# Performance work log

Hardware: AMD Instinct MI355X
Metric: run time of the kernel (lower is better)

The kernel has to match this reference:

```python
import jax, jax.numpy as jnp
import numpy as np

B, S, D = 32, 2048, 8
H = 256
COUPLING = -1.0  # TC['WOBBLE_COUPLING'] default
WOBBLE_STEP = 0.03125


def setup_inputs() -> dict:
    key = jax.random.key(0)
    k = jax.random.split(key, 5)
    return {
        'x': jax.random.normal(k[0], (B, S, D), dtype=jnp.float32),
        'We': jax.random.normal(k[1], (H, D), dtype=jnp.float32) * 0.35,
        'be': jax.random.normal(k[2], (H,), dtype=jnp.float32) * 0.02,
        'Wr': jax.random.normal(k[3], (256, 7 * H), dtype=jnp.float32) * 0.02,
        'br': jax.random.normal(k[4], (256,), dtype=jnp.float32) * 0.02,
    }


def _forward(x, We, be, Wr, br):
    Bm, Sm, _ = x.shape
    h = We.shape[0]

    def step(carry, xt):
        ph, wb, prev_xt, has_prev = carry
        pt = xt @ We.T + be                      # [B,h] embedded phase increments
        # xpt = stack([cos(pt), sin(pt)]); accumulator consumes the spinor pair,
        # equivalent to the wrapped phase delta atan2(sin, cos)
        delta = jnp.arctan2(jnp.sin(pt), jnp.cos(pt))
        wb2 = wb + WOBBLE_STEP
        is_rep = has_prev * jnp.all(xt == prev_xt, axis=1, keepdims=True).astype(x.dtype)
        # WobblePhaseAccumulator(spinor=True): phase advances by delta plus
        # coupling-modulated wobble; wobble channel accumulates delta
        ph_out = ph + delta + COUPLING * jnp.sin(wb2)
        wb_out = wb2 + delta
        ph_new = ph_out
        wb_new = is_rep * wb_out + (1.0 - is_rep) * wb2
        ph_s = 0.5 * ph_new
        readout = jnp.concatenate([
            jnp.cos(ph_new), jnp.sin(ph_new),
            jnp.cos(ph_s), jnp.sin(ph_s),
            jnp.cos(wb_new), jnp.sin(wb_new),
            ph_new,
        ], axis=1)                                # [B, 7h]
        logits = readout @ Wr.T + br              # [B, 256]
        return (ph_new, wb_new, xt, jnp.ones((), x.dtype)), (logits, ph_new, wb_new)

    ph0 = jnp.zeros((Bm, h), x.dtype)
    wb0 = jnp.zeros((Bm, h), x.dtype)
    prev0 = jnp.zeros((Bm, x.shape[2]), x.dtype)
    carry0 = (ph0, wb0, prev0, jnp.zeros((), x.dtype))
    xs = jnp.swapaxes(x, 0, 1)                    # [S,B,D]
    _, (logits, ph_hist, wb_hist) = jax.lax.scan(step, carry0, xs)
    logits = jnp.swapaxes(logits, 0, 1)           # [B,S,256]
    ph_hist = jnp.swapaxes(ph_hist, 0, 1)         # [B,S,h]
    wb_hist = jnp.swapaxes(wb_hist, 0, 1)         # [B,S,h]
    return logits, ph_hist, wb_hist


def reference(x, We, be, Wr, br):
    return _forward(x, We, be, Wr, br)
```

## Files before the change

### kernel.cpp

```cpp
#include <hip/hip_runtime.h>
#include <hip/hip_bf16.h>
#include <math.h>

#define NB 32
#define NS 2048
#define ND 8
#define NH 256
#define NK 1792
#define NO 256
#define NM (NB*NS)
#define WSTEP 0.03125f
#define CCH 64
#define LCH (NS/CCH)

typedef __attribute__((ext_vector_type(8))) short short8;
typedef __attribute__((ext_vector_type(4))) float f32x4;

__device__ float g_ssum[NB*CCH*NH];
__device__ float g_wb0 [NB*CCH*NH];
__device__ float g_esum[NB*CCH*NH];
__device__ float g_ph0 [NB*CCH*NH];
__device__ float g_rep [NB*NS];
__device__ unsigned short g_bb[NO*NK];

__device__ __forceinline__ unsigned short bf16_rn(float f){
    union { float f; unsigned int u; } v; v.f = f;
    unsigned int u = v.u;
    unsigned int r = (u + 0x7FFFu + ((u >> 16) & 1u)) >> 16;
    return (unsigned short)r;
}

extern "C" __global__ __launch_bounds__(256)
void k_delta(const float* __restrict__ x, const float* __restrict__ We,
             const float* __restrict__ be, float* __restrict__ delta){
    int blk = blockIdx.x;
    int b = blk >> 6;
    int c = blk & (CCH-1);
    int t0 = c * LCH;
    int h = threadIdx.x;
    __shared__ float xs[(LCH+1)*ND];
    __shared__ float rep[LCH];

    for(int i = h; i < (LCH+1)*ND/4; i += 256){
        int row  = i >> 1;
        int col4 = (i & 1) * 4;
        int t = t0 - 1 + row; if(t < 0) t = 0;
        *(float4*)&xs[row*ND + col4] = *(const float4*)&x[((size_t)b*NS + t)*ND + col4];
    }
    __syncthreads();
    if(h < LCH){
        int t = t0 + h;
        float fl = 0.f;
        if(t > 0){
            bool eq = true;
            #pragma unroll
            for(int d2 = 0; d2 < ND; ++d2) eq = eq && (xs[(h+1)*ND+d2] == xs[h*ND+d2]);
            fl = eq ? 1.f : 0.f;
        }
        rep[h] = fl;
        g_rep[b*NS + t] = fl;
    }
    __syncthreads();

    float4 w0 = *(const float4*)&We[h*ND];
    float4 w1 = *(const float4*)&We[h*ND + 4];
    float bh = be[h];
    float ssum = 0.f;
    for(int j = 0; j < LCH; ++j){
        const float* xr = &xs[(j+1)*ND];
        float pt = bh + xr[0]*w0.x + xr[1]*w0.y + xr[2]*w0.z + xr[3]*w0.w
                      + xr[4]*w1.x + xr[5]*w1.y + xr[6]*w1.z + xr[7]*w1.w;
        float s, cc;
        sincosf(pt, &s, &cc);
        float d = atan2f(s, cc);
        delta[((size_t)(t0+j)*NB + b)*NH + h] = d;
        ssum += WSTEP + rep[j]*d;
    }
    g_ssum[(b*CCH + c)*NH + h] = ssum;
}

extern "C" __global__ __launch_bounds__(256)
void k_prefix_s(){
    int g = blockIdx.x*256 + threadIdx.x;
    int b = g >> 8, h = g & 255;
    float acc = 0.f;
    for(int c = 0; c < CCH; ++c){
        size_t idx = ((size_t)(b*CCH + c))*NH + h;
        g_wb0[idx] = acc;
        acc += g_ssum[idx];
    }
}
extern "C" __global__ __launch_bounds__(256)
void k_prefix_e(){
    int g = blockIdx.x*256 + threadIdx.x;
    int b = g >> 8, h = g & 255;
    float acc = 0.f;
    for(int c = 0; c < CCH; ++c){
        size_t idx = ((size_t)(b*CCH + c))*NH + h;
        g_ph0[idx] = acc;
        acc += g_esum[idx];
    }
}

extern "C" __global__ __launch_bounds__(256)
void k_escan(const float* __restrict__ delta, float* __restrict__ wb_hist){
    int blk = blockIdx.x;
    int b = blk >> 6, c = blk & (CCH-1), t0 = c*LCH, h = threadIdx.x;
    __shared__ float rep[LCH];
    if(h < LCH) rep[h] = g_rep[b*NS + t0 + h];
    __syncthreads();
    float wb = g_wb0[(b*CCH + c)*NH + h];
    const float* dp = delta + (size_t)t0*NB*NH + b*NH + h;
    float* wp = wb_hist + ((size_t)b*NS + t0)*NH + h;
    float d[LCH];
    #pragma unroll
    for(int j = 0; j < LCH; ++j) d[j] = dp[(size_t)j*(NB*NH)];
    float esum = 0.f;
    #pragma unroll
    for(int j = 0; j < LCH; ++j){
        float wb2 = wb + WSTEP;
        float e = d[j] - sinf(wb2);
        esum += e;
        wb = wb2 + rep[j]*d[j];
        wp[(size_t)j*NH] = wb;
    }
    g_esum[(b*CCH + c)*NH + h] = esum;
}

extern "C" __global__ __launch_bounds__(256)
void k_phw(const float* __restrict__ delta, float* __restrict__ ph_hist){
    int blk = blockIdx.x;
    int b = blk >> 6, c = blk & (CCH-1), t0 = c*LCH, h = threadIdx.x;
    __shared__ float rep[LCH];
    if(h < LCH) rep[h] = g_rep[b*NS + t0 + h];
    __syncthreads();
    float wb = g_wb0[(b*CCH + c)*NH + h];
    float ph = g_ph0[(b*CCH + c)*NH + h];
    const float* dp = delta + (size_t)t0*NB*NH + b*NH + h;
    float* pp = ph_hist + ((size_t)b*NS + t0)*NH + h;
    float d[LCH];
    #pragma unroll
    for(int j = 0; j < LCH; ++j) d[j] = dp[(size_t)j*(NB*NH)];
    #pragma unroll
    for(int j = 0; j < LCH; ++j){
        float wb2 = wb + WSTEP;
        float e = d[j] - sinf(wb2);
        ph += e;
        wb = wb2 + rep[j]*d[j];
        pp[(size_t)j*NH] = ph;
    }
}

extern "C" __global__ __launch_bounds__(256)
void k_bconv(const float* __restrict__ Wr){
    int i = (blockIdx.x*256 + threadIdx.x) * 8;
    if(i >= NO*NK) return;
    float4 a = *(const float4*)&Wr[i];
    float4 b = *(const float4*)&Wr[i+4];
    union { unsigned int u[4]; uint4 v; } r;
    r.u[0] = (unsigned int)bf16_rn(a.x) | ((unsigned int)bf16_rn(a.y) << 16);
    r.u[1] = (unsigned int)bf16_rn(a.z) | ((unsigned int)bf16_rn(a.w) << 16);
    r.u[2] = (unsigned int)bf16_rn(b.x) | ((unsigned int)bf16_rn(b.y) << 16);
    r.u[3] = (unsigned int)bf16_rn(b.z) | ((unsigned int)bf16_rn(b.w) << 16);
    *(uint4*)&g_bb[i] = r.v;
}

extern "C" __global__ __launch_bounds__(512, 4)
void k_logits(const float* __restrict__ ph_hist, const float* __restrict__ wb_hist,
              const float* __restrict__ br, float* __restrict__ logits){
    __shared__ __align__(16) unsigned short Al[128][40];
    int tid  = threadIdx.x;
    int m0   = blockIdx.x * 128;
    int lane = tid & 63, wid = tid >> 6;
    int wm = wid >> 2, wn = wid & 3;
    int l15 = lane & 15, kg = lane >> 4;
    int colb = wn*64 + l15;
    int arow = tid >> 2, ah = (tid & 3) * 8;

    f32x4 acc[4][4];
    f32x4 zz = {0.f, 0.f, 0.f, 0.f};
    #pragma unroll
    for(int i = 0; i < 4; ++i)
        #pragma unroll
        for(int j = 0; j < 4; ++j) acc[i][j] = zz;

    for(int ks = 0; ks < 56; ++ks){
        int c    = ks >> 3;
        int kcol = (ks & 7) * 32;

        const float* src = (c == 4 || c == 5) ? wb_hist : ph_hist;
        const float* p = src + (size_t)(m0 + arow)*NH + kcol + ah;
        float4 x0 = *(const float4*)p;
        float4 x1 = *(const float4*)(p + 4);
        float v[8] = {x0.x, x0.y, x0.z, x0.w, x1.x, x1.y, x1.z, x1.w};
        if(c != 6){
            float sc = (c == 2 || c == 3) ? 0.07957747154594767f
                                          : 0.15915494309189535f;
            bool is_sin = (c & 1);
            #pragma unroll
            for(int j = 0; j < 8; ++j){
                float r = v[j] * sc;
                r -= floorf(r);
                v[j] = is_sin ? __builtin_amdgcn_sinf(r) : __builtin_amdgcn_cosf(r);
            }
        }
        union { unsigned int u[4]; uint4 q; } pk;
        #pragma unroll
        for(int j = 0; j < 4; ++j)
            asm("v_cvt_pk_bf16_f32 %0, %1, %2"
                : "=v"(pk.u[j]) : "v"(v[2*j]), "v"(v[2*j+1]));

        short8 bfr[4];
        #pragma unroll
        for(int nf = 0; nf < 4; ++nf)
            bfr[nf] = *(const short8*)&g_bb[(size_t)(colb + nf*16)*NK + c*256 + kcol + kg*8];

        __syncthreads();
        *(uint4*)&Al[arow][ah] = pk.q;
        __syncthreads();

        short8 afr[4];
        #pragma unroll
        for(int mf = 0; mf < 4; ++mf)
            afr[mf] = *(const short8*)&Al[wm*64 + mf*16 + l15][kg*8];
        #pragma unroll
        for(int mf = 0; mf < 4; ++mf)
            #pragma unroll
            for(int nf = 0; nf < 4; ++nf)
                acc[mf][nf] = __builtin_amdgcn_mfma_f32_16x16x32_bf16(
                    afr[mf], bfr[nf], acc[mf][nf], 0, 0, 0);
    }

    #pragma unroll
    for(int nf = 0; nf < 4; ++nf){
        int col = wn*64 + nf*16 + l15;
        float bias = br[col];
        #pragma unroll
        for(int mf = 0; mf < 4; ++mf){
            int row = m0 + wm*64 + mf*16 + kg*4;
            #pragma unroll
            for(int r = 0; r < 4; ++r)
                logits[(size_t)(row + r)*NO + col] = acc[mf][nf][r] + bias;
        }
    }
}

extern "C" void kernel_launch(void* const* d_in, const int* in_sizes, int n_in,
                              void* d_out, int out_size, void* d_ws, size_t ws_size,
                              hipStream_t stream){
    const float* x  = (const float*)d_in[0];
    const float* We = (const float*)d_in[1];
    const float* be = (const float*)d_in[2];
    const float* Wr = (const float*)d_in[3];
    const float* br = (const float*)d_in[4];

    float* logits = (float*)d_out;
    float* ph     = logits + (size_t)NM*NO;
    float* wb     = ph + (size_t)NM*NH;
    float* delta  = logits;

    hipLaunchKernelGGL(k_bconv,    dim3((NO*NK/8 + 255)/256), dim3(256), 0, stream, Wr);
    hipLaunchKernelGGL(k_delta,    dim3(NB*CCH), dim3(256), 0, stream, x, We, be, delta);
    hipLaunchKernelGGL(k_prefix_s, dim3(32),     dim3(256), 0, stream);
    hipLaunchKernelGGL(k_escan,    dim3(NB*CCH), dim3(256), 0, stream, delta, wb);
    hipLaunchKernelGGL(k_prefix_e, dim3(32),     dim3(256), 0, stream);
    hipLaunchKernelGGL(k_phw,      dim3(NB*CCH), dim3(256), 0, stream, delta, ph);
    hipLaunchKernelGGL(k_logits,   dim3(NM/128), dim3(512), 0, stream, ph, wb, br, logits);
}
```

Baseline: 415.4 us.

## Fuse readout feature build per h-slice and use double-angle identities

The logits kernel now loops over 8 h-slices instead of 56 k-steps. Each slice loads ph and wb once, computes sin/cos of ph/2 and derives cos/sin of ph with double-angle identities, then writes all 7 feature blocks to a wider LDS tile before running the MFMAs. This cuts redundant global reloads of ph_hist (four reads per element become one), halves the transcendental count for the ph features, and drops barriers from 112 to 16 per block. In exchange LDS use per block grows and register pressure rises, which may reduce occupancy under the (512,4) launch bounds. The double-angle values also round slightly differently from direct evaluation.

New measurement: 400.8 us. 1.04x faster.

```diff
diff --git a/kernel.cpp b/kernel.cpp
--- a/kernel.cpp
+++ b/kernel.cpp
@@ -165,17 +165,18 @@
     *(uint4*)&g_bb[i] = r.v;
 }
 
+#define LSTR 232
 extern "C" __global__ __launch_bounds__(512, 4)
 void k_logits(const float* __restrict__ ph_hist, const float* __restrict__ wb_hist,
               const float* __restrict__ br, float* __restrict__ logits){
-    __shared__ __align__(16) unsigned short Al[128][40];
+    __shared__ __align__(16) unsigned short Al[128][LSTR];
     int tid  = threadIdx.x;
     int m0   = blockIdx.x * 128;
     int lane = tid & 63, wid = tid >> 6;
     int wm = wid >> 2, wn = wid & 3;
     int l15 = lane & 15, kg = lane >> 4;
     int colb = wn*64 + l15;
-    int arow = tid >> 2, ah = (tid & 3) * 8;
+    int arow = tid >> 2, aq = (tid & 3) * 8;
 
     f32x4 acc[4][4];
     f32x4 zz = {0.f, 0.f, 0.f, 0.f};
@@ -184,51 +185,81 @@
         #pragma unroll
         for(int j = 0; j < 4; ++j) acc[i][j] = zz;
 
-    for(int ks = 0; ks < 56; ++ks){
-        int c    = ks >> 3;
-        int kcol = (ks & 7) * 32;
-
-        const float* src = (c == 4 || c == 5) ? wb_hist : ph_hist;
-        const float* p = src + (size_t)(m0 + arow)*NH + kcol + ah;
-        float4 x0 = *(const float4*)p;
-        float4 x1 = *(const float4*)(p + 4);
-        float v[8] = {x0.x, x0.y, x0.z, x0.w, x1.x, x1.y, x1.z, x1.w};
-        if(c != 6){
-            float sc = (c == 2 || c == 3) ? 0.07957747154594767f
-                                          : 0.15915494309189535f;
-            bool is_sin = (c & 1);
-            #pragma unroll
-            for(int j = 0; j < 8; ++j){
-                float r = v[j] * sc;
-                r -= floorf(r);
-                v[j] = is_sin ? __builtin_amdgcn_sinf(r) : __builtin_amdgcn_cosf(r);
-            }
-        }
-        union { unsigned int u[4]; uint4 q; } pk;
+    for(int hs = 0; hs < 8; ++hs){
+        int hb = hs*32 + aq;
+        const float* pp = ph_hist + (size_t)(m0 + arow)*NH + hb;
+        const float* pw = wb_hist + (size_t)(m0 + arow)*NH + hb;
+        float4 a0 = *(const float4*)pp;
+        float4 a1 = *(const float4*)(pp + 4);
+        float4 b0 = *(const float4*)pw;
+        float4 b1 = *(const float4*)(pw + 4);
+        float v[8] = {a0.x,a0.y,a0.z,a0.w, a1.x,a1.y,a1.z,a1.w};
+        float w[8] = {b0.x,b0.y,b0.z,b0.w, b1.x,b1.y,b1.z,b1.w};
+
+        unsigned int pk[7][4];
+        float s2[8], c2[8];
         #pragma unroll
         for(int j = 0; j < 4; ++j)
-            asm("v_cvt_pk_bf16_f32 %0, %1, %2"
-                : "=v"(pk.u[j]) : "v"(v[2*j]), "v"(v[2*j+1]));
-
-        short8 bfr[4];
-        #pragma unroll
-        for(int nf = 0; nf < 4; ++nf)
-            bfr[nf] = *(const short8*)&g_bb[(size_t)(colb + nf*16)*NK + c*256 + kcol + kg*8];
+            asm("v_cvt_pk_bf16_f32 %0, %1, %2" : "=v"(pk[6][j]) : "v"(v[2*j]), "v"(v[2*j+1]));
+        #pragma unroll
+        for(int j = 0; j < 8; ++j){
+            float r = v[j] * 0.07957747154594767f;
+            r -= floorf(r);
+            s2[j] = __builtin_amdgcn_sinf(r);
+            c2[j] = __builtin_amdgcn_cosf(r);
+        }
+        #pragma unroll
+        for(int j = 0; j < 4; ++j){
+            asm("v_cvt_pk_bf16_f32 %0, %1, %2" : "=v"(pk[2][j]) : "v"(c2[2*j]), "v"(c2[2*j+1]));
+            asm("v_cvt_pk_bf16_f32 %0, %1, %2" : "=v"(pk[3][j]) : "v"(s2[2*j]), "v"(s2[2*j+1]));
+        }
+        #pragma unroll
+        for(int j = 0; j < 8; ++j){
+            float cv = (c2[j]-s2[j])*(c2[j]+s2[j]);
+            float sv = 2.f*s2[j]*c2[j];
+            s2[j] = cv; c2[j] = sv;
+        }
+        #pragma unroll
+        for(int j = 0; j < 4; ++j){
+            asm("v_cvt_pk_bf16_f32 %0, %1, %2" : "=v"(pk[0][j]) : "v"(s2[2*j]), "v"(s2[2*j+1]));
+            asm("v_cvt_pk_bf16_f32 %0, %1, %2" : "=v"(pk[1][j]) : "v"(c2[2*j]), "v"(c2[2*j+1]));
+        }
+        #pragma unroll
+        for(int j = 0; j < 8; ++j){
+            float r = w[j] * 0.15915494309189535f;
+            r -= floorf(r);
+            s2[j] = __builtin_amdgcn_sinf(r);
+            c2[j] = __builtin_amdgcn_cosf(r);
+        }
+        #pragma unroll
+        for(int j = 0; j < 4; ++j){
+            asm("v_cvt_pk_bf16_f32 %0, %1, %2" : "=v"(pk[4][j]) : "v"(c2[2*j]), "v"(c2[2*j+1]));
+            asm("v_cvt_pk_bf16_f32 %0, %1, %2" : "=v"(pk[5][j]) : "v"(s2[2*j]), "v"(s2[2*j+1]));
+        }
 
         __syncthreads();
-        *(uint4*)&Al[arow][ah] = pk.q;
+        #pragma unroll
+        for(int c = 0; c < 7; ++c)
+            *(uint4*)&Al[arow][c*32 + aq] = make_uint4(pk[c][0], pk[c][1], pk[c][2], pk[c][3]);
         __syncthreads();
 
-        short8 afr[4];
-        #pragma unroll
-        for(int mf = 0; mf < 4; ++mf)
-            afr[mf] = *(const short8*)&Al[wm*64 + mf*16 + l15][kg*8];
-        #pragma unroll
-        for(int mf = 0; mf < 4; ++mf)
+        #pragma unroll
+        for(int c = 0; c < 7; ++c){
+            short8 bfr[4];
             #pragma unroll
             for(int nf = 0; nf < 4; ++nf)
-                acc[mf][nf] = __builtin_amdgcn_mfma_f32_16x16x32_bf16(
-                    afr[mf], bfr[nf], acc[mf][nf], 0, 0, 0);
+                bfr[nf] = *(const short8*)&g_bb[(size_t)(colb + nf*16)*NK + c*256 + hs*32 + kg*8];
+            short8 afr[4];
+            #pragma unroll
+            for(int mf = 0; mf < 4; ++mf)
+                afr[mf] = *(const short8*)&Al[wm*64 + mf*16 + l15][c*32 + kg*8];
+            #pragma unroll
+            for(int mf = 0; mf < 4; ++mf)
+                #pragma unroll
+                for(int nf = 0; nf < 4; ++nf)
+                    acc[mf][nf] = __builtin_amdgcn_mfma_f32_16x16x32_bf16(
+                        afr[mf], bfr[nf], acc[mf][nf], 0, 0, 0);
+        }
     }
 
     #pragma unroll
```
